# Kernel optimization log

Measured on AMD Instinct MI355X. Metric: run time of the kernel, lower is better.

The kernel has to match this reference:

```python
import jax, jax.numpy as jnp
import numpy as np
from jax import lax

SPARSE_TH = 0.01
STRIDE = (1, 1)


def setup_inputs() -> dict:
    key = jax.random.key(0)
    k1, k2, k3 = jax.random.split(key, 3)
    x = jax.random.normal(k1, (32, 56, 56, 256), dtype=jnp.float32)  # NHWC
    # weight: (out_channels, in_channels, kh, kw); scale so a fraction falls below sparse_th
    weight = jax.random.normal(k2, (256, 256, 3, 3), dtype=jnp.float32) * 0.05
    bias = jax.random.normal(k3, (256,), dtype=jnp.float32)
    return {"x": x, "weight": weight, "bias": bias}


def reference(x, weight, bias):
    # Threshold weights: |w| < sparse_th -> 0 (the sparse kernel computes the
    # identical math as a dense valid conv with the masked weight)
    w = jnp.where(jnp.abs(weight) < SPARSE_TH, jnp.zeros_like(weight), weight)
    # OIHW -> HWIO for NHWC conv
    w_hwio = jnp.transpose(w, (2, 3, 1, 0))
    out = lax.conv_general_dilated(
        x, w_hwio,
        window_strides=STRIDE,
        padding="VALID",
        dimension_numbers=("NHWC", "HWIO", "NHWC"),
    )
    return out + bias.reshape(1, 1, 1, -1)
```

## Files before the change

kernel.cpp:

```cpp
#include <hip/hip_runtime.h>
#include <hip/hip_bf16.h>


typedef __bf16 bf16x8 __attribute__((ext_vector_type(8)));
typedef float f32x4 __attribute__((ext_vector_type(4)));

#define GLOBAL_AS __attribute__((address_space(1)))
#define LDS_AS __attribute__((address_space(3)))

static __device__ __forceinline__ void glds16(const void* g, void* l) {
    __builtin_amdgcn_global_load_lds((const GLOBAL_AS unsigned int*)g,
                                     (LDS_AS unsigned int*)l, 16, 0, 0);
}

static __device__ __forceinline__ unsigned short f2bf(float f) {
    unsigned int u = __float_as_uint(f);
    unsigned int r = u + 0x7FFFu + ((u >> 16) & 1u);
    return (unsigned short)(r >> 16);
}

__global__ void cvt_xw(const float* __restrict__ x, unsigned short* __restrict__ xb,
                       const float* __restrict__ w, unsigned short* __restrict__ wt) {
    const int NXB = 32 * 56 * 56 * 256 / (256 * 8);
    if (blockIdx.x < NXB) {
        int i = (blockIdx.x * 256 + threadIdx.x) * 8;
        const float4* p = (const float4*)(x + i);
        float4 a = p[0], b = p[1];
        uint4 v;
        v.x = (unsigned)f2bf(a.x) | ((unsigned)f2bf(a.y) << 16);
        v.y = (unsigned)f2bf(a.z) | ((unsigned)f2bf(a.w) << 16);
        v.z = (unsigned)f2bf(b.x) | ((unsigned)f2bf(b.y) << 16);
        v.w = (unsigned)f2bf(b.z) | ((unsigned)f2bf(b.w) << 16);
        *(uint4*)(xb + i) = v;
    } else {
        int co = blockIdx.x - NXB;
        int ci = threadIdx.x;
        const float* src = w + co * 2304 + ci * 9;
        unsigned short* dst = wt + co * 2304 + ci;
#pragma unroll
        for (int khw = 0; khw < 9; ++khw) {
            float v = src[khw];
            v = (fabsf(v) < 0.01f) ? 0.0f : v;
            dst[khw * 256] = f2bf(v);
        }
    }
}

static __device__ __forceinline__ int swz_key(int row16) {
    return (row16 & 3) ^ ((row16 >> 2) & 3);
}

__global__ __launch_bounds__(256) void conv_gemm(
    const unsigned short* __restrict__ Xb,
    const unsigned short* __restrict__ Wt,
    const float* __restrict__ bias,
    float* __restrict__ Out)
{
    __shared__ __align__(16) unsigned short As[2][128 * 32];
    __shared__ __align__(16) unsigned short Bs[2][128 * 32];

    const int tid  = threadIdx.x;
    const int lane = tid & 63;
    const int wave = tid >> 6;

    const int bx = blockIdx.x;
    const int xcd = bx & 7;
    const int slt = bx >> 3;
    const int v   = xcd * 182 + (xcd < 2 ? xcd : 2) + slt;
    const int m0  = (v >> 1) * 128;
    const int co0 = (v & 1) * 128;

    const int srow = lane >> 2;
    const int schunk_g = (lane & 3) ^ swz_key(srow);
    const int scol = schunk_g * 8;

    const unsigned short* a_src[2];
    const unsigned short* b_src[2];
#pragma unroll
    for (int r = 0; r < 2; ++r) {
        int row = r * 64 + wave * 16 + srow;
        int m = m0 + row;
        int n = m / 2916;
        int rem = m - n * 2916;
        int oh = rem / 54;
        int ow = rem - oh * 54;
        a_src[r] = Xb + (((n * 56 + oh) * 56 + ow) << 8) + scol;
        b_src[r] = Wt + (co0 + row) * 2304 + scol;
    }

    const int fm = lane & 15;
    const int fq = lane >> 4;
    const int wm = (wave >> 1) * 64;
    const int wn = (wave & 1) * 64;
    const int slot8 = (fq ^ swz_key(fm)) * 8;

    f32x4 acc[4][4];
#pragma unroll
    for (int i = 0; i < 4; ++i)
#pragma unroll
        for (int j = 0; j < 4; ++j)
            acc[i][j] = (f32x4){0.f, 0.f, 0.f, 0.f};

#pragma unroll
    for (int r = 0; r < 2; ++r) {
        glds16(a_src[r], &As[0][wave * 512 + r * 2048]);
        glds16(b_src[r], &Bs[0][wave * 512 + r * 2048]);
    }

#pragma unroll 1
    for (int kc = 0; kc < 72; ++kc) {
        __syncthreads();

        if (kc < 71) {
            const int kcn = kc + 1;
            const int khwn = kcn >> 3;
            const int khn = (khwn * 11) >> 5;
            const int kwn = khwn - khn * 3;
            const int aoffn = ((khn * 56 + kwn) << 8) + (kcn & 7) * 32;
            const int boffn = kcn * 32;
            const int b = kcn & 1;
#pragma unroll
            for (int r = 0; r < 2; ++r) {
                glds16(a_src[r] + aoffn, &As[b][wave * 512 + r * 2048]);
                glds16(b_src[r] + boffn, &Bs[b][wave * 512 + r * 2048]);
            }
        }

        const unsigned short* Ab = As[kc & 1];
        const unsigned short* Bb = Bs[kc & 1];
        bf16x8 af[4], bfr[4];
#pragma unroll
        for (int mi = 0; mi < 4; ++mi)
            af[mi] = *(const bf16x8*)&Ab[(wm + mi * 16 + fm) * 32 + slot8];
#pragma unroll
        for (int ni = 0; ni < 4; ++ni)
            bfr[ni] = *(const bf16x8*)&Bb[(wn + ni * 16 + fm) * 32 + slot8];
#pragma unroll
        for (int mi = 0; mi < 4; ++mi)
#pragma unroll
            for (int ni = 0; ni < 4; ++ni)
                acc[mi][ni] = __builtin_amdgcn_mfma_f32_16x16x32_bf16(
                    af[mi], bfr[ni], acc[mi][ni], 0, 0, 0);
    }

    float bv[4];
#pragma unroll
    for (int ni = 0; ni < 4; ++ni) bv[ni] = bias[co0 + wn + ni * 16 + fm];
#pragma unroll
    for (int mi = 0; mi < 4; ++mi) {
#pragma unroll
        for (int reg = 0; reg < 4; ++reg) {
            int m = m0 + wm + mi * 16 + fq * 4 + reg;
            float* orow = Out + m * 256 + co0 + wn + fm;
#pragma unroll
            for (int ni = 0; ni < 4; ++ni)
                orow[ni * 16] = acc[mi][ni][reg] + bv[ni];
        }
    }
}

extern "C" void kernel_launch(void* const* d_in, const int* in_sizes, int n_in,
                              void* d_out, int out_size, void* d_ws, size_t ws_size,
                              hipStream_t stream) {
    const float* x    = (const float*)d_in[0];
    const float* w    = (const float*)d_in[1];
    const float* bias = (const float*)d_in[2];
    float* out = (float*)d_out;

    const int NX = 32 * 56 * 56 * 256;
    unsigned short* xb = (unsigned short*)d_ws;
    unsigned short* wt = xb + NX;

    cvt_xw<<<NX / (256 * 8) + 256, 256, 0, stream>>>(x, xb, w, wt);
    conv_gemm<<<729 * 2, 256, 0, stream>>>(xb, wt, bias, out);
}
```

Baseline: 301.8 us.

## Widen conv GEMM tile to full 256 channels with 4-stage LDS pipeline

Each block now computes a 128x256 output tile with 8 waves, covering all output channels, so the im2col A tile is loaded once instead of twice. Loads are issued three stages ahead into a 4-deep LDS ring buffer, with explicit vmcnt waits and barriers replacing the per-iteration __syncthreads. MFMA sections run under raised wave priority. The XCD-aware block remapping is dropped, and the larger LDS footprint (96KB) may limit occupancy.

```diff
diff --git a/kernel.cpp b/kernel.cpp
--- a/kernel.cpp
+++ b/kernel.cpp
@@ -50,48 +50,42 @@
     return (row16 & 3) ^ ((row16 >> 2) & 3);
 }
 
-__global__ __launch_bounds__(256) void conv_gemm(
+__global__ __launch_bounds__(512, 2) void conv_gemm(
     const unsigned short* __restrict__ Xb,
     const unsigned short* __restrict__ Wt,
     const float* __restrict__ bias,
     float* __restrict__ Out)
 {
-    __shared__ __align__(16) unsigned short As[2][128 * 32];
-    __shared__ __align__(16) unsigned short Bs[2][128 * 32];
+    __shared__ __align__(16) unsigned short As[4][128 * 32];
+    __shared__ __align__(16) unsigned short Bs[4][256 * 32];
 
     const int tid  = threadIdx.x;
     const int lane = tid & 63;
     const int wave = tid >> 6;
 
-    const int bx = blockIdx.x;
-    const int xcd = bx & 7;
-    const int slt = bx >> 3;
-    const int v   = xcd * 182 + (xcd < 2 ? xcd : 2) + slt;
-    const int m0  = (v >> 1) * 128;
-    const int co0 = (v & 1) * 128;
+    const int m0 = blockIdx.x * 128;
 
-    const int srow = lane >> 2;
-    const int schunk_g = (lane & 3) ^ swz_key(srow);
-    const int scol = schunk_g * 8;
+    const int arow = tid >> 2;
+    const int ach  = (tid & 3) ^ swz_key(arow & 15);
+    int am = m0 + arow;
+    int an = am / 2916;
+    int arem = am - an * 2916;
+    int aoh = arem / 54;
+    int aow = arem - aoh * 54;
+    const unsigned short* a_base =
+        Xb + (((an * 56 + aoh) * 56 + aow) << 8) + ach * 8;
 
-    const unsigned short* a_src[2];
-    const unsigned short* b_src[2];
-#pragma unroll
-    for (int r = 0; r < 2; ++r) {
-        int row = r * 64 + wave * 16 + srow;
-        int m = m0 + row;
-        int n = m / 2916;
-        int rem = m - n * 2916;
-        int oh = rem / 54;
-        int ow = rem - oh * 54;
-        a_src[r] = Xb + (((n * 56 + oh) * 56 + ow) << 8) + scol;
-        b_src[r] = Wt + (co0 + row) * 2304 + scol;
-    }
+    const int s1 = 512 + tid;
+    const int br0 = tid >> 2, br1 = s1 >> 2;
+    const unsigned short* b_base0 =
+        Wt + br0 * 2304 + (((tid & 3) ^ swz_key(br0 & 15)) << 3);
+    const unsigned short* b_base1 =
+        Wt + br1 * 2304 + (((s1 & 3) ^ swz_key(br1 & 15)) << 3);
 
     const int fm = lane & 15;
     const int fq = lane >> 4;
-    const int wm = (wave >> 1) * 64;
-    const int wn = (wave & 1) * 64;
+    const int wm = (wave >> 2) * 64;
+    const int wn = (wave & 3) * 64;
     const int slot8 = (fq ^ swz_key(fm)) * 8;
 
     f32x4 acc[4][4];
@@ -102,32 +96,18 @@
             acc[i][j] = (f32x4){0.f, 0.f, 0.f, 0.f};
 
 #pragma unroll
-    for (int r = 0; r < 2; ++r) {
-        glds16(a_src[r], &As[0][wave * 512 + r * 2048]);
-        glds16(b_src[r], &Bs[0][wave * 512 + r * 2048]);
+    for (int tp = 0; tp < 3; ++tp) {
+        glds16(a_base + tp * 32, &As[tp][wave * 512]);
+        glds16(b_base0 + tp * 32, &Bs[tp][wave * 512]);
+        glds16(b_base1 + tp * 32, &Bs[tp][4096 + wave * 512]);
     }
+    asm volatile("s_waitcnt vmcnt(6)\n\ts_barrier" ::: "memory");
 
 #pragma unroll 1
-    for (int kc = 0; kc < 72; ++kc) {
-        __syncthreads();
-
-        if (kc < 71) {
-            const int kcn = kc + 1;
-            const int khwn = kcn >> 3;
-            const int khn = (khwn * 11) >> 5;
-            const int kwn = khwn - khn * 3;
-            const int aoffn = ((khn * 56 + kwn) << 8) + (kcn & 7) * 32;
-            const int boffn = kcn * 32;
-            const int b = kcn & 1;
-#pragma unroll
-            for (int r = 0; r < 2; ++r) {
-                glds16(a_src[r] + aoffn, &As[b][wave * 512 + r * 2048]);
-                glds16(b_src[r] + boffn, &Bs[b][wave * 512 + r * 2048]);
-            }
-        }
-
-        const unsigned short* Ab = As[kc & 1];
-        const unsigned short* Bb = Bs[kc & 1];
+    for (int t = 0; t < 72; ++t) {
+        const int b = t & 3;
+        const unsigned short* Ab = As[b];
+        const unsigned short* Bb = Bs[b];
         bf16x8 af[4], bfr[4];
 #pragma unroll
         for (int mi = 0; mi < 4; ++mi)
@@ -135,23 +115,42 @@
 #pragma unroll
         for (int ni = 0; ni < 4; ++ni)
             bfr[ni] = *(const bf16x8*)&Bb[(wn + ni * 16 + fm) * 32 + slot8];
+
+        const int tn = t + 3;
+        if (tn < 72) {
+            const int bn = tn & 3;
+            const int khw = tn >> 3;
+            const int kh = (khw * 11) >> 5;
+            const int kw = khw - kh * 3;
+            const int aoff = ((kh * 56 + kw) << 8) + (tn & 7) * 32;
+            const int boff = tn * 32;
+            glds16(a_base + aoff, &As[bn][wave * 512]);
+            glds16(b_base0 + boff, &Bs[bn][wave * 512]);
+            glds16(b_base1 + boff, &Bs[bn][4096 + wave * 512]);
+        }
+
+        __builtin_amdgcn_s_setprio(1);
 #pragma unroll
         for (int mi = 0; mi < 4; ++mi)
 #pragma unroll
             for (int ni = 0; ni < 4; ++ni)
                 acc[mi][ni] = __builtin_amdgcn_mfma_f32_16x16x32_bf16(
                     af[mi], bfr[ni], acc[mi][ni], 0, 0, 0);
+        __builtin_amdgcn_s_setprio(0);
+
+        if (t < 69) asm volatile("s_waitcnt vmcnt(6)\n\ts_barrier" ::: "memory");
+        else        asm volatile("s_waitcnt vmcnt(0)\n\ts_barrier" ::: "memory");
     }
 
     float bv[4];
 #pragma unroll
-    for (int ni = 0; ni < 4; ++ni) bv[ni] = bias[co0 + wn + ni * 16 + fm];
+    for (int ni = 0; ni < 4; ++ni) bv[ni] = bias[wn + ni * 16 + fm];
 #pragma unroll
     for (int mi = 0; mi < 4; ++mi) {
 #pragma unroll
         for (int reg = 0; reg < 4; ++reg) {
             int m = m0 + wm + mi * 16 + fq * 4 + reg;
-            float* orow = Out + m * 256 + co0 + wn + fm;
+            float* orow = Out + m * 256 + wn + fm;
 #pragma unroll
             for (int ni = 0; ni < 4; ++ni)
                 orow[ni * 16] = acc[mi][ni][reg] + bv[ni];
@@ -172,5 +171,5 @@
     unsigned short* wt = xb + NX;
 
     cvt_xw<<<NX / (256 * 8) + 256, 256, 0, stream>>>(x, xb, w, wt);
-    conv_gemm<<<729 * 2, 256, 0, stream>>>(xb, wt, bias, out);
+    conv_gemm<<<729, 512, 0, stream>>>(xb, wt, bias, out);
 }
```

New measurement: 299.5 us. About the same (-0.8%).
